# Optimization experiments

Measured on AMD Instinct MI355X. Metric: run time of the kernel, lower is better.

Reference implementation:

```python
import jax, jax.numpy as jnp
import numpy as np
from jax import lax

B, T, I, H, L = 64, 2048, 128, 256, 2
P = 0.25  # dropouto


def _lstm_layer(x, W_ih, W_hh, b_ih, b_hh):
    """Single LSTM layer. x: [B,T,in]. Torch gate order: i, f, g, o."""
    # Precompute input projection for all timesteps (one big GEMM).
    xW = jnp.einsum('bti,gi->btg', x, W_ih) + b_ih + b_hh  # [B,T,4H]
    h0 = jnp.zeros((x.shape[0], W_hh.shape[1]), x.dtype)
    c0 = jnp.zeros_like(h0)

    def step(carry, xw_t):
        h, c = carry
        g = xw_t + h @ W_hh.T  # [B,4H]
        i, f, gg, o = jnp.split(g, 4, axis=-1)
        c = jax.nn.sigmoid(f) * c + jax.nn.sigmoid(i) * jnp.tanh(gg)
        h = jax.nn.sigmoid(o) * jnp.tanh(c)
        return (h, c), h

    (hT, cT), hs = lax.scan(step, (h0, c0), xW.transpose(1, 0, 2))
    return hs.transpose(1, 0, 2), hT, cT  # [B,T,H], [B,H], [B,H]


def setup_inputs() -> dict:
    key = jax.random.key(0)
    ks = jax.random.split(key, 16)
    s = 1.0 / np.sqrt(H)
    inp = {'x': jax.random.normal(ks[0], (B, T, I), jnp.float32)}
    for l in range(L):
        d_in = I if l == 0 else H
        inp[f'W_ih{l}'] = jax.random.uniform(ks[1 + 4 * l], (4 * H, d_in), jnp.float32, -s, s)
        inp[f'W_hh{l}'] = jax.random.uniform(ks[2 + 4 * l], (4 * H, H), jnp.float32, -s, s)
        inp[f'b_ih{l}'] = jax.random.uniform(ks[3 + 4 * l], (4 * H,), jnp.float32, -s, s)
        inp[f'b_hh{l}'] = jax.random.uniform(ks[4 + 4 * l], (4 * H,), jnp.float32, -s, s)
        # variational dropout mask on layer output: same mask for every timestep
        keep = jax.random.bernoulli(ks[9 + l], 1.0 - P, (B, H))
        inp[f'mask{l}'] = keep.astype(jnp.float32) / (1.0 - P)
    return inp


def reference(x, W_ih0, W_hh0, b_ih0, b_hh0, W_ih1, W_hh1, b_ih1, b_hh1, mask0, mask1):
    params = [(W_ih0, W_hh0, b_ih0, b_hh0, mask0), (W_ih1, W_hh1, b_ih1, b_hh1, mask1)]
    h_ns, c_ns = [], []
    out = x
    for (W_ih, W_hh, b_ih, b_hh, mask) in params:
        out, hT, cT = _lstm_layer(out, W_ih, W_hh, b_ih, b_hh)
        out = out * mask[:, None, :]  # variational dropouto (shared over time)
        h_ns.append(hT)
        c_ns.append(cT)
    h_n = jnp.stack(h_ns, axis=0)  # [L,B,H]
    c_n = jnp.stack(c_ns, axis=0)
    return out, (h_n, c_n)
```

## Files before the change

### kernel.cpp

```cpp
#include <hip/hip_runtime.h>

#define B_  64
#define T_  2048
#define I_  128
#define H_  256
#define G4  1024
#define TC  128

#define HC  16
#define MC  9
#define SC  7

typedef float    f32x4 __attribute__((ext_vector_type(4)));
typedef _Float16 f16x8 __attribute__((ext_vector_type(8)));
typedef _Float16 f16x2 __attribute__((ext_vector_type(2)));

__device__ __forceinline__ float dot2f(unsigned w, unsigned h, float acc) {
#if __has_builtin(__builtin_amdgcn_fdot2)
  return __builtin_amdgcn_fdot2(__builtin_bit_cast(f16x2, w),
                                __builtin_bit_cast(f16x2, h), acc, false);
#else
  f16x2 a = __builtin_bit_cast(f16x2, w), b = __builtin_bit_cast(f16x2, h);
  return acc + (float)a[0] * (float)b[0] + (float)a[1] * (float)b[1];
#endif
}

__device__ __forceinline__ unsigned short h16bits(float f) {
  return __builtin_bit_cast(unsigned short, (_Float16)f);
}
__device__ __forceinline__ float sigm(float x) { return 1.f / (1.f + __expf(-x)); }
__device__ __forceinline__ float tanh_fast(float x) { return 2.f / (1.f + __expf(-2.f * x)) - 1.f; }


__global__ void prep_w(const float* __restrict__ Whh, uint4* __restrict__ wall) {
  int idx = blockIdx.x * 256 + threadIdx.x;
  if (idx >= 32 * 1024) return;
  int c4 = idx >> 10, r = idx & 1023;
  unsigned q[4];
#pragma unroll
  for (int m = 0; m < 4; m++) {
    int kd = 4 * c4 + m;
    unsigned lo = h16bits(Whh[r * 256 + 2 * kd]);
    unsigned hi = h16bits(Whh[r * 256 + 2 * kd + 1]);
    q[m] = lo | (hi << 16);
  }
  wall[c4 * 1024 + r] = make_uint4(q[0], q[1], q[2], q[3]);
}

__global__ void prep_f16(const float* __restrict__ src, _Float16* __restrict__ dst, int n) {
  int i = blockIdx.x * 256 + threadIdx.x;
  if (i < n) dst[i] = (_Float16)src[i];
}

__global__ void prep_bias(const float* __restrict__ bi, const float* __restrict__ bh,
                          float* __restrict__ bias) {
  int i = blockIdx.x * 256 + threadIdx.x;
  if (i < G4) bias[i] = bi[i] + bh[i];
}

template <int K, bool SRC_F32>
__global__ __launch_bounds__(256) void proj_kernel(const void* __restrict__ Asrc,
                                                   const _Float16* __restrict__ Wf,
                                                   const float* __restrict__ bias,
                                                   _Float16* __restrict__ xw, int t0) {
  const int m  = blockIdx.x;
  const int n0 = blockIdx.y * 64;
  const int tid = threadIdx.x;
  const int lane = tid & 63, wv = tid >> 6;

  __shared__ _Float16 As[64][40];
  __shared__ _Float16 Bs[64][40];

  f32x4 acc[4] = {f32x4{0,0,0,0}, f32x4{0,0,0,0}, f32x4{0,0,0,0}, f32x4{0,0,0,0}};

  const int r  = tid >> 2;
  const int kq = (tid & 3) * 8;
  const int r_g = m * 64 + r;
  const int b  = r_g >> 7;
  const int tc = r_g & (TC - 1);
  long arow;
  if (SRC_F32) arow = (long)(b * T_ + t0 + tc) * K;
  else         arow = (long)r_g * K;

  for (int k0 = 0; k0 < K; k0 += 32) {
    if (SRC_F32) {
      const float* ap = (const float*)Asrc + arow + k0 + kq;
      float4 a0 = *(const float4*)ap;
      float4 a1 = *(const float4*)(ap + 4);
      _Float16* d = &As[r][kq];
      d[0] = (_Float16)a0.x; d[1] = (_Float16)a0.y; d[2] = (_Float16)a0.z; d[3] = (_Float16)a0.w;
      d[4] = (_Float16)a1.x; d[5] = (_Float16)a1.y; d[6] = (_Float16)a1.z; d[7] = (_Float16)a1.w;
    } else {
      const _Float16* ap = (const _Float16*)Asrc + arow + k0 + kq;
      *(uint4*)&As[r][kq] = *(const uint4*)ap;
    }
    *(uint4*)&Bs[r][kq] = *(const uint4*)(Wf + (long)(n0 + r) * K + k0 + kq);
    __syncthreads();

    f16x8 av = *(const f16x8*)&As[wv * 16 + (lane & 15)][(lane >> 4) * 8];
#pragma unroll
    for (int q = 0; q < 4; q++) {
      f16x8 bv = *(const f16x8*)&Bs[q * 16 + (lane & 15)][(lane >> 4) * 8];
      acc[q] = __builtin_amdgcn_mfma_f32_16x16x32_f16(av, bv, acc[q], 0, 0, 0);
    }
    __syncthreads();
  }

  const int row_in = wv * 16 + ((lane >> 4) << 2);
  const int col_in = lane & 15;
#pragma unroll
  for (int q = 0; q < 4; q++) {
#pragma unroll
    for (int i = 0; i < 4; i++) {
      int rr = m * 64 + row_in + i;
      int cc = n0 + q * 16 + col_in;
      xw[(long)rr * G4 + cc] = (_Float16)(acc[q][i] + bias[cc]);
    }
  }
}


struct ScanJob {
  const _Float16* xw;
  const uint4*    wall;
  const float*    mask;
  float* hstate; float* cstate;
  _Float16* ychunk;
  float* out;
  float* hn; float* cn;
  int t0; int valid;
};

#define C16(X) X(0) X(1) X(2) X(3) X(4) X(5) X(6) X(7) \
               X(8) X(9) X(10) X(11) X(12) X(13) X(14) X(15)

#define LOADW(i) \
  uint4 wA_##i = wall[(i) * 1024 + r0]; \
  uint4 wB_##i = wall[(i) * 1024 + r1];

#define PINW(i) \
  asm volatile("" : "+v"(wA_##i.x), "+v"(wA_##i.y), "+v"(wA_##i.z), "+v"(wA_##i.w), \
                    "+v"(wB_##i.x), "+v"(wB_##i.y), "+v"(wB_##i.z), "+v"(wB_##i.w));

#define DOTW(i) { uint4 hv = hs4[i]; \
  accA0 = dot2f(wA_##i.x, hv.x, accA0); accB0 = dot2f(wB_##i.x, hv.x, accB0); \
  accA1 = dot2f(wA_##i.y, hv.y, accA1); accB1 = dot2f(wB_##i.y, hv.y, accB1); \
  accA0 = dot2f(wA_##i.z, hv.z, accA0); accB0 = dot2f(wB_##i.z, hv.z, accB0); \
  accA1 = dot2f(wA_##i.w, hv.w, accA1); accB1 = dot2f(wB_##i.w, hv.w, accB1); }

__global__ __launch_bounds__(512)
__attribute__((amdgpu_waves_per_eu(2, 2)))
void scan_kernel(ScanJob j0, ScanJob j1) {
  ScanJob j = (blockIdx.x < B_) ? j0 : j1;
  if (!j.valid) return;
  const int b = blockIdx.x & (B_ - 1);
  const int t = threadIdx.x;
  const int p = t & 255, s = t >> 8;
  const int r0 = p + s * 256;
  const int r1 = r0 + 512;

  __shared__ uint4 wmid[MC * 1024];
  __shared__ __align__(16) unsigned short hsm[256];
  __shared__ float pig[256];

  const uint4* wall = j.wall;

#pragma unroll
  for (int i = 0; i < MC * 2; i++)
    wmid[i * 512 + t] = wall[HC * 1024 + i * 512 + t];

  C16(LOADW)
  C16(PINW)

  float c_reg = 0.f, h_reg = 0.f, mk = 0.f;
  if (s == 1) {
    c_reg = j.cstate[b * 256 + p];
    mk    = j.mask[b * 256 + p];
  }
  if (t < 128) {
    float h0v = j.hstate[b * 256 + 2 * t];
    float h1v = j.hstate[b * 256 + 2 * t + 1];
    ((unsigned*)hsm)[t] = (unsigned)h16bits(h0v) | ((unsigned)h16bits(h1v) << 16);
  }
  __syncthreads();

  const uint4* hs4 = (const uint4*)hsm;
  const _Float16* xwb = j.xw + (long)b * TC * G4;
  float xA = (float)xwb[r0], xB = (float)xwb[r1];
  float hm_prev = 0.f;

  for (int tc = 0; tc < TC; ++tc) {
    float nA = 0.f, nB = 0.f;
    if (tc + 1 < TC) {
      nA = (float)xwb[(long)(tc + 1) * G4 + r0];
      nB = (float)xwb[(long)(tc + 1) * G4 + r1];
    }

    if (s == 1 && tc > 0) {
      if (j.ychunk) j.ychunk[(b * TC + tc - 1) * H_ + p] = (_Float16)hm_prev;
      else          j.out[(long)(b * T_ + j.t0 + tc - 1) * H_ + p] = hm_prev;
    }

    float accA0 = xA, accA1 = 0.f, accB0 = xB, accB1 = 0.f;

    {
      const uint4* wsp = wall + (HC + MC) * 1024;
      asm volatile("" : "+v"(wsp));
#pragma unroll
      for (int m = 0; m < SC; m++) {
        uint4 hv = hs4[HC + MC + m];
        uint4 gA = wsp[m * 1024 + r0];
        uint4 gB = wsp[m * 1024 + r1];
        accA0 = dot2f(gA.x, hv.x, accA0); accB0 = dot2f(gB.x, hv.x, accB0);
        accA1 = dot2f(gA.y, hv.y, accA1); accB1 = dot2f(gB.y, hv.y, accB1);
        accA0 = dot2f(gA.z, hv.z, accA0); accB0 = dot2f(gB.z, hv.z, accB0);
        accA1 = dot2f(gA.w, hv.w, accA1); accB1 = dot2f(gB.w, hv.w, accB1);
      }
    }

    C16(DOTW)

#pragma unroll
    for (int m = 0; m < MC; m++) {
      uint4 hv = hs4[HC + m];
      uint4 tA = wmid[m * 1024 + r0];
      uint4 tB = wmid[m * 1024 + r1];
      accA0 = dot2f(tA.x, hv.x, accA0); accB0 = dot2f(tB.x, hv.x, accB0);
      accA1 = dot2f(tA.y, hv.y, accA1); accB1 = dot2f(tB.y, hv.y, accB1);
      accA0 = dot2f(tA.z, hv.z, accA0); accB0 = dot2f(tB.z, hv.z, accB0);
      accA1 = dot2f(tA.w, hv.w, accA1); accB1 = dot2f(tB.w, hv.w, accB1);
    }

    float aF = accA0 + accA1;
    float bF = accB0 + accB1;

    if (s == 0) pig[p] = sigm(aF) * tanh_fast(bF);
    __syncthreads();
    if (s == 1) {
      c_reg = sigm(aF) * c_reg + pig[p];
      h_reg = sigm(bF) * tanh_fast(c_reg);
      hsm[p] = h16bits(h_reg);
      hm_prev = h_reg * mk;
    }
    xA = nA; xB = nB;
    __syncthreads();
  }

  if (s == 1) {
    if (j.ychunk) j.ychunk[(b * TC + TC - 1) * H_ + p] = (_Float16)hm_prev;
    else          j.out[(long)(b * T_ + j.t0 + TC - 1) * H_ + p] = hm_prev;
    j.hstate[b * 256 + p] = h_reg;
    j.cstate[b * 256 + p] = c_reg;
    if (j.hn) { j.hn[b * 256 + p] = h_reg; j.cn[b * 256 + p] = c_reg; }
  }
}

extern "C" void kernel_launch(void* const* d_in, const int* in_sizes, int n_in,
                              void* d_out, int out_size, void* d_ws, size_t ws_size,
                              hipStream_t stream) {
  const float* x     = (const float*)d_in[0];
  const float* Wih0  = (const float*)d_in[1];
  const float* Whh0  = (const float*)d_in[2];
  const float* bih0  = (const float*)d_in[3];
  const float* bhh0  = (const float*)d_in[4];
  const float* mask0 = (const float*)d_in[5];
  const float* Wih1  = (const float*)d_in[6];
  const float* Whh1  = (const float*)d_in[7];
  const float* bih1  = (const float*)d_in[8];
  const float* bhh1  = (const float*)d_in[9];
  const float* mask1 = (const float*)d_in[10];

  float* out = (float*)d_out;
  float* hn  = out + (long)B_ * T_ * H_;
  float* cn  = hn + 2 * B_ * H_;

  char* w = (char*)d_ws;
  uint4*    wall0  = (uint4*)w;      w += 512 << 10;
  uint4*    wall1  = (uint4*)w;      w += 512 << 10;
  _Float16* wf0    = (_Float16*)w;   w += 256 << 10;
  _Float16* wf1    = (_Float16*)w;   w += 512 << 10;
  float*    bias0  = (float*)w;      w += 4 << 10;
  float*    bias1  = (float*)w;      w += 4 << 10;
  float*    h0s    = (float*)w;      w += 64 << 10;
  float*    c0s    = (float*)w;      w += 64 << 10;
  float*    h1s    = (float*)w;      w += 64 << 10;
  float*    c1s    = (float*)w;      w += 64 << 10;
  _Float16* xw0    = (_Float16*)w;   w += (long)B_ * TC * G4 * 2;
  _Float16* xw1    = (_Float16*)w;   w += (long)B_ * TC * G4 * 2;
  _Float16* ybuf   = (_Float16*)w;   w += (long)B_ * TC * H_ * 2;

  hipMemsetAsync(h0s, 0, 4 * (64 << 10), stream);

  prep_w<<<128, 256, 0, stream>>>(Whh0, wall0);
  prep_w<<<128, 256, 0, stream>>>(Whh1, wall1);
  prep_f16<<<512, 256, 0, stream>>>(Wih0, wf0, G4 * I_);
  prep_f16<<<1024, 256, 0, stream>>>(Wih1, wf1, G4 * H_);
  prep_bias<<<4, 256, 0, stream>>>(bih0, bhh0, bias0);
  prep_bias<<<4, 256, 0, stream>>>(bih1, bhh1, bias1);

  const int nchunk = T_ / TC;
  for (int k = 0; k <= nchunk; k++) {
    if (k < nchunk) {
      proj_kernel<I_, true><<<dim3(B_ * TC / 64, G4 / 64), 256, 0, stream>>>(
          x, wf0, bias0, xw0, k * TC);
    }
    ScanJob j0, j1;
    j0.xw = xw0; j0.wall = wall0; j0.mask = mask0;
    j0.hstate = h0s; j0.cstate = c0s;
    j0.ychunk = ybuf; j0.out = nullptr;
    j0.hn = (k == nchunk - 1) ? hn : nullptr;
    j0.cn = (k == nchunk - 1) ? cn : nullptr;
    j0.t0 = k * TC; j0.valid = (k < nchunk);
    j1.xw = xw1; j1.wall = wall1; j1.mask = mask1;
    j1.hstate = h1s; j1.cstate = c1s;
    j1.ychunk = nullptr; j1.out = out;
    j1.hn = (k == nchunk) ? hn + B_ * H_ : nullptr;
    j1.cn = (k == nchunk) ? cn + B_ * H_ : nullptr;
    j1.t0 = (k - 1) * TC; j1.valid = (k >= 1);

    scan_kernel<<<2 * B_, 512, 0, stream>>>(j0, j1);

    if (k < nchunk) {
      proj_kernel<H_, false><<<dim3(B_ * TC / 64, G4 / 64), 256, 0, stream>>>(
          ybuf, wf1, bias1, xw1, k * TC);
    }
  }
}
```

Baseline: 6.372 ms.

## Process two batch rows per scan block to share recurrent weight loads

Each scan block now runs the recurrence for two batch rows at once, so every weight fragment it loads is used against two hidden-state vectors. The grid is halved to one block per batch pair. The weight split also changes: fewer chunks stay pinned in registers (HC from 16 to 8) and more are streamed from global memory, interleaved with software-prefetched loads. The trade is more arithmetic and more global/L2 weight traffic per timestep on each block, with only half as many CUs active, in exchange for reusing each weight across two batches.

```diff
diff --git a/kernel.cpp b/kernel.cpp
--- a/kernel.cpp
+++ b/kernel.cpp
@@ -7,9 +7,8 @@
 #define G4  1024
 #define TC  128
 
-#define HC  16
+#define HC  8
 #define MC  9
-#define SC  7
 
 typedef float    f32x4 __attribute__((ext_vector_type(4)));
 typedef _Float16 f16x8 __attribute__((ext_vector_type(8)));
@@ -131,127 +130,152 @@
   int t0; int valid;
 };
 
-#define C16(X) X(0) X(1) X(2) X(3) X(4) X(5) X(6) X(7) \
-               X(8) X(9) X(10) X(11) X(12) X(13) X(14) X(15)
+#define C8(X) X(0) X(1) X(2) X(3) X(4) X(5) X(6) X(7)
 
 #define LOADW(i) \
-  uint4 wA_##i = wall[(i) * 1024 + r0]; \
-  uint4 wB_##i = wall[(i) * 1024 + r1];
+  uint4 wA_##i = wall_p[(i) * 1024 + r0]; \
+  uint4 wB_##i = wall_p[(i) * 1024 + r1];
 
 #define PINW(i) \
   asm volatile("" : "+v"(wA_##i.x), "+v"(wA_##i.y), "+v"(wA_##i.z), "+v"(wA_##i.w), \
                     "+v"(wB_##i.x), "+v"(wB_##i.y), "+v"(wB_##i.z), "+v"(wB_##i.w));
 
-#define DOTW(i) { uint4 hv = hs4[i]; \
-  accA0 = dot2f(wA_##i.x, hv.x, accA0); accB0 = dot2f(wB_##i.x, hv.x, accB0); \
-  accA1 = dot2f(wA_##i.y, hv.y, accA1); accB1 = dot2f(wB_##i.y, hv.y, accB1); \
-  accA0 = dot2f(wA_##i.z, hv.z, accA0); accB0 = dot2f(wB_##i.z, hv.z, accB0); \
-  accA1 = dot2f(wA_##i.w, hv.w, accA1); accB1 = dot2f(wB_##i.w, hv.w, accB1); }
-
-__global__ __launch_bounds__(512)
-__attribute__((amdgpu_waves_per_eu(2, 2)))
-void scan_kernel(ScanJob j0, ScanJob j1) {
-  ScanJob j = (blockIdx.x < B_) ? j0 : j1;
+#define DOT2T(gA, gB, c) { uint4 hv0 = hsA[c]; uint4 hv1 = hsB[c]; \
+  a00 = dot2f(gA.x, hv0.x, a00); a10 = dot2f(gA.x, hv1.x, a10); \
+  a01 = dot2f(gB.x, hv0.x, a01); a11 = dot2f(gB.x, hv1.x, a11); \
+  a00 = dot2f(gA.y, hv0.y, a00); a10 = dot2f(gA.y, hv1.y, a10); \
+  a01 = dot2f(gB.y, hv0.y, a01); a11 = dot2f(gB.y, hv1.y, a11); \
+  a00 = dot2f(gA.z, hv0.z, a00); a10 = dot2f(gA.z, hv1.z, a10); \
+  a01 = dot2f(gB.z, hv0.z, a01); a11 = dot2f(gB.z, hv1.z, a11); \
+  a00 = dot2f(gA.w, hv0.w, a00); a10 = dot2f(gA.w, hv1.w, a10); \
+  a01 = dot2f(gB.w, hv0.w, a01); a11 = dot2f(gB.w, hv1.w, a11); }
+
+#define DOTR(i)   DOT2T(wA_##i, wB_##i, i)
+#define DOTL(c)   { uint4 tA = wmid[((c) - HC) * 1024 + r0]; \
+                    uint4 tB = wmid[((c) - HC) * 1024 + r1]; \
+                    DOT2T(tA, tB, c) }
+#define LOADS(n, c) uint4 sA_##n = wsp[((c) - HC - MC) * 1024 + r0]; \
+                    uint4 sB_##n = wsp[((c) - HC - MC) * 1024 + r1];
+#define DOTS(n, c)  DOT2T(sA_##n, sB_##n, c)
+
+__global__ __launch_bounds__(512, 1) void scan_kernel(ScanJob j0, ScanJob j1) {
+  const int nb = gridDim.x >> 1;
+  ScanJob j = (blockIdx.x < nb) ? j0 : j1;
   if (!j.valid) return;
-  const int b = blockIdx.x & (B_ - 1);
+  const int bb = (blockIdx.x < nb) ? blockIdx.x : blockIdx.x - nb;
+  const int b0 = 2 * bb, b1 = 2 * bb + 1;
   const int t = threadIdx.x;
-  const int p = t & 255, s = t >> 8;
-  const int r0 = p + s * 256;
-  const int r1 = r0 + 512;
+  const int r0 = t, r1 = t + 512;
+  const int s = t >> 8, jj = t & 255;
 
   __shared__ uint4 wmid[MC * 1024];
-  __shared__ __align__(16) unsigned short hsm[256];
-  __shared__ float pig[256];
-
-  const uint4* wall = j.wall;
+  __shared__ __align__(16) unsigned short hsm[2][256];
+  __shared__ float pig[2][256];
+
+  const uint4* wall_p = j.wall;
 
 #pragma unroll
   for (int i = 0; i < MC * 2; i++)
-    wmid[i * 512 + t] = wall[HC * 1024 + i * 512 + t];
-
-  C16(LOADW)
-  C16(PINW)
-
-  float c_reg = 0.f, h_reg = 0.f, mk = 0.f;
+    wmid[i * 512 + t] = wall_p[HC * 1024 + i * 512 + t];
+
+  C8(LOADW)
+  C8(PINW)
+
+  float c0 = 0.f, c1 = 0.f, h0 = 0.f, h1 = 0.f, mk0 = 0.f, mk1 = 0.f;
   if (s == 1) {
-    c_reg = j.cstate[b * 256 + p];
-    mk    = j.mask[b * 256 + p];
-  }
-  if (t < 128) {
-    float h0v = j.hstate[b * 256 + 2 * t];
-    float h1v = j.hstate[b * 256 + 2 * t + 1];
-    ((unsigned*)hsm)[t] = (unsigned)h16bits(h0v) | ((unsigned)h16bits(h1v) << 16);
+    c0  = j.cstate[b0 * 256 + jj];
+    c1  = j.cstate[b1 * 256 + jj];
+    mk0 = j.mask[b0 * 256 + jj];
+    mk1 = j.mask[b1 * 256 + jj];
+    hsm[1][jj] = h16bits(j.hstate[b1 * 256 + jj]);
+  } else {
+    hsm[0][jj] = h16bits(j.hstate[b0 * 256 + jj]);
   }
   __syncthreads();
 
-  const uint4* hs4 = (const uint4*)hsm;
-  const _Float16* xwb = j.xw + (long)b * TC * G4;
-  float xA = (float)xwb[r0], xB = (float)xwb[r1];
-  float hm_prev = 0.f;
+  const uint4* hsA = (const uint4*)hsm[0];
+  const uint4* hsB = (const uint4*)hsm[1];
+  const _Float16* xwb0 = j.xw + (long)b0 * TC * G4;
+  const _Float16* xwb1 = j.xw + (long)b1 * TC * G4;
+  float x00 = (float)xwb0[r0], x01 = (float)xwb0[r1];
+  float x10 = (float)xwb1[r0], x11 = (float)xwb1[r1];
+  float hm0p = 0.f, hm1p = 0.f;
 
   for (int tc = 0; tc < TC; ++tc) {
-    float nA = 0.f, nB = 0.f;
+    float n00 = 0.f, n01 = 0.f, n10 = 0.f, n11 = 0.f;
     if (tc + 1 < TC) {
-      nA = (float)xwb[(long)(tc + 1) * G4 + r0];
-      nB = (float)xwb[(long)(tc + 1) * G4 + r1];
+      const long nx = (long)(tc + 1) * G4;
+      n00 = (float)xwb0[nx + r0]; n01 = (float)xwb0[nx + r1];
+      n10 = (float)xwb1[nx + r0]; n11 = (float)xwb1[nx + r1];
     }
 
     if (s == 1 && tc > 0) {
-      if (j.ychunk) j.ychunk[(b * TC + tc - 1) * H_ + p] = (_Float16)hm_prev;
-      else          j.out[(long)(b * T_ + j.t0 + tc - 1) * H_ + p] = hm_prev;
-    }
-
-    float accA0 = xA, accA1 = 0.f, accB0 = xB, accB1 = 0.f;
-
-    {
-      const uint4* wsp = wall + (HC + MC) * 1024;
-      asm volatile("" : "+v"(wsp));
-#pragma unroll
-      for (int m = 0; m < SC; m++) {
-        uint4 hv = hs4[HC + MC + m];
-        uint4 gA = wsp[m * 1024 + r0];
-        uint4 gB = wsp[m * 1024 + r1];
-        accA0 = dot2f(gA.x, hv.x, accA0); accB0 = dot2f(gB.x, hv.x, accB0);
-        accA1 = dot2f(gA.y, hv.y, accA1); accB1 = dot2f(gB.y, hv.y, accB1);
-        accA0 = dot2f(gA.z, hv.z, accA0); accB0 = dot2f(gB.z, hv.z, accB0);
-        accA1 = dot2f(gA.w, hv.w, accA1); accB1 = dot2f(gB.w, hv.w, accB1);
+      if (j.ychunk) {
+        j.ychunk[(b0 * TC + tc - 1) * H_ + jj] = (_Float16)hm0p;
+        j.ychunk[(b1 * TC + tc - 1) * H_ + jj] = (_Float16)hm1p;
+      } else {
+        j.out[(long)(b0 * T_ + j.t0 + tc - 1) * H_ + jj] = hm0p;
+        j.out[(long)(b1 * T_ + j.t0 + tc - 1) * H_ + jj] = hm1p;
       }
     }
 
-    C16(DOTW)
-
-#pragma unroll
-    for (int m = 0; m < MC; m++) {
-      uint4 hv = hs4[HC + m];
-      uint4 tA = wmid[m * 1024 + r0];
-      uint4 tB = wmid[m * 1024 + r1];
-      accA0 = dot2f(tA.x, hv.x, accA0); accB0 = dot2f(tB.x, hv.x, accB0);
-      accA1 = dot2f(tA.y, hv.y, accA1); accB1 = dot2f(tB.y, hv.y, accB1);
-      accA0 = dot2f(tA.z, hv.z, accA0); accB0 = dot2f(tB.z, hv.z, accB0);
-      accA1 = dot2f(tA.w, hv.w, accA1); accB1 = dot2f(tB.w, hv.w, accB1);
-    }
-
-    float aF = accA0 + accA1;
-    float bF = accB0 + accB1;
-
-    if (s == 0) pig[p] = sigm(aF) * tanh_fast(bF);
+    float a00 = x00, a01 = x01, a10 = x10, a11 = x11;
+
+    const uint4* wsp = wall_p + (HC + MC) * 1024;
+    asm volatile("" : "+v"(wsp));
+
+    LOADS(0, 17) LOADS(1, 18) LOADS(2, 19) LOADS(3, 20)
+    C8(DOTR)
+    DOTS(0, 17) DOTS(1, 18)
+
+    LOADS(4, 21) LOADS(5, 22) LOADS(6, 23) LOADS(7, 24)
+    DOTS(2, 19) DOTS(3, 20)
+    DOTL(8) DOTL(9) DOTL(10)
+    DOTS(4, 21) DOTS(5, 22)
+
+    LOADS(8, 25) LOADS(9, 26) LOADS(10, 27) LOADS(11, 28)
+    DOTS(6, 23) DOTS(7, 24)
+    DOTL(11) DOTL(12) DOTL(13)
+    DOTS(8, 25) DOTS(9, 26)
+
+    LOADS(12, 29) LOADS(13, 30) LOADS(14, 31)
+    DOTS(10, 27) DOTS(11, 28)
+    DOTL(14) DOTL(15) DOTL(16)
+    DOTS(12, 29) DOTS(13, 30) DOTS(14, 31)
+
+    if (s == 0) {
+      pig[0][jj] = sigm(a00) * tanh_fast(a01);
+      pig[1][jj] = sigm(a10) * tanh_fast(a11);
+    }
     __syncthreads();
     if (s == 1) {
-      c_reg = sigm(aF) * c_reg + pig[p];
-      h_reg = sigm(bF) * tanh_fast(c_reg);
-      hsm[p] = h16bits(h_reg);
-      hm_prev = h_reg * mk;
-    }
-    xA = nA; xB = nB;
+      c0 = sigm(a00) * c0 + pig[0][jj];
+      h0 = sigm(a01) * tanh_fast(c0);
+      hsm[0][jj] = h16bits(h0);
+      hm0p = h0 * mk0;
+      c1 = sigm(a10) * c1 + pig[1][jj];
+      h1 = sigm(a11) * tanh_fast(c1);
+      hsm[1][jj] = h16bits(h1);
+      hm1p = h1 * mk1;
+    }
+    x00 = n00; x01 = n01; x10 = n10; x11 = n11;
     __syncthreads();
   }
 
   if (s == 1) {
-    if (j.ychunk) j.ychunk[(b * TC + TC - 1) * H_ + p] = (_Float16)hm_prev;
-    else          j.out[(long)(b * T_ + j.t0 + TC - 1) * H_ + p] = hm_prev;
-    j.hstate[b * 256 + p] = h_reg;
-    j.cstate[b * 256 + p] = c_reg;
-    if (j.hn) { j.hn[b * 256 + p] = h_reg; j.cn[b * 256 + p] = c_reg; }
+    if (j.ychunk) {
+      j.ychunk[(b0 * TC + TC - 1) * H_ + jj] = (_Float16)hm0p;
+      j.ychunk[(b1 * TC + TC - 1) * H_ + jj] = (_Float16)hm1p;
+    } else {
+      j.out[(long)(b0 * T_ + j.t0 + TC - 1) * H_ + jj] = hm0p;
+      j.out[(long)(b1 * T_ + j.t0 + TC - 1) * H_ + jj] = hm1p;
+    }
+    j.hstate[b0 * 256 + jj] = h0; j.cstate[b0 * 256 + jj] = c0;
+    j.hstate[b1 * 256 + jj] = h1; j.cstate[b1 * 256 + jj] = c1;
+    if (j.hn) {
+      j.hn[b0 * 256 + jj] = h0; j.cn[b0 * 256 + jj] = c0;
+      j.hn[b1 * 256 + jj] = h1; j.cn[b1 * 256 + jj] = c1;
+    }
   }
 }
 
@@ -318,7 +342,7 @@
     j1.cn = (k == nchunk) ? cn + B_ * H_ : nullptr;
     j1.t0 = (k - 1) * TC; j1.valid = (k >= 1);
 
-    scan_kernel<<<2 * B_, 512, 0, stream>>>(j0, j1);
+    scan_kernel<<<B_, 512, 0, stream>>>(j0, j1);
 
     if (k < nchunk) {
       proj_kernel<H_, false><<<dim3(B_ * TC / 64, G4 / 64), 256, 0, stream>>>(
```

Result: slower. 9.039 ms (+41.9%).

## Keep 23 weight chunks in registers, drop per-step global weight streaming

Applied to the files above, without the earlier changes.

Moves the seven recurrent-weight chunks that were re-read from global or L2 memory every timestep into registers, growing the register-resident set from 16 to 23 uint4 pairs. Launch bounds change to one block per CU, replacing the waves-per-EU hint so the larger register budget is allowed. The goal is to remove per-step global loads from the serial recurrence critical path. The risk is register pressure and spilling, since each thread now pins 184 VGPRs of weights.

```diff
diff --git a/kernel.cpp b/kernel.cpp
--- a/kernel.cpp
+++ b/kernel.cpp
@@ -7,9 +7,8 @@
 #define G4  1024
 #define TC  128
 
-#define HC  16
+#define HC  23
 #define MC  9
-#define SC  7
 
 typedef float    f32x4 __attribute__((ext_vector_type(4)));
 typedef _Float16 f16x8 __attribute__((ext_vector_type(8)));
@@ -131,26 +130,26 @@
   int t0; int valid;
 };
 
-#define C16(X) X(0) X(1) X(2) X(3) X(4) X(5) X(6) X(7) \
-               X(8) X(9) X(10) X(11) X(12) X(13) X(14) X(15)
+#define C23(X) X(0) X(1) X(2) X(3) X(4) X(5) X(6) X(7) X(8) X(9) X(10) X(11) \
+               X(12) X(13) X(14) X(15) X(16) X(17) X(18) X(19) X(20) X(21) X(22)
 
 #define LOADW(i) \
-  uint4 wA_##i = wall[(i) * 1024 + r0]; \
-  uint4 wB_##i = wall[(i) * 1024 + r1];
+  uint4 wA_##i = wall_p[(i) * 1024 + r0]; \
+  uint4 wB_##i = wall_p[(i) * 1024 + r1];
 
 #define PINW(i) \
   asm volatile("" : "+v"(wA_##i.x), "+v"(wA_##i.y), "+v"(wA_##i.z), "+v"(wA_##i.w), \
                     "+v"(wB_##i.x), "+v"(wB_##i.y), "+v"(wB_##i.z), "+v"(wB_##i.w));
 
-#define DOTW(i) { uint4 hv = hs4[i]; \
-  accA0 = dot2f(wA_##i.x, hv.x, accA0); accB0 = dot2f(wB_##i.x, hv.x, accB0); \
-  accA1 = dot2f(wA_##i.y, hv.y, accA1); accB1 = dot2f(wB_##i.y, hv.y, accB1); \
-  accA0 = dot2f(wA_##i.z, hv.z, accA0); accB0 = dot2f(wB_##i.z, hv.z, accB0); \
-  accA1 = dot2f(wA_##i.w, hv.w, accA1); accB1 = dot2f(wB_##i.w, hv.w, accB1); }
-
-__global__ __launch_bounds__(512)
-__attribute__((amdgpu_waves_per_eu(2, 2)))
-void scan_kernel(ScanJob j0, ScanJob j1) {
+#define DOT2(gA, gB, c) { uint4 hv = hs4[c]; \
+  a0 = dot2f(gA.x, hv.x, a0); a1 = dot2f(gB.x, hv.x, a1); \
+  b0 = dot2f(gA.y, hv.y, b0); b1 = dot2f(gB.y, hv.y, b1); \
+  a0 = dot2f(gA.z, hv.z, a0); a1 = dot2f(gB.z, hv.z, a1); \
+  b0 = dot2f(gA.w, hv.w, b0); b1 = dot2f(gB.w, hv.w, b1); }
+
+#define DOTR(i)  DOT2(wA_##i, wB_##i, i)
+
+__global__ __launch_bounds__(512, 1) void scan_kernel(ScanJob j0, ScanJob j1) {
   ScanJob j = (blockIdx.x < B_) ? j0 : j1;
   if (!j.valid) return;
   const int b = blockIdx.x & (B_ - 1);
@@ -163,24 +162,21 @@
   __shared__ __align__(16) unsigned short hsm[256];
   __shared__ float pig[256];
 
-  const uint4* wall = j.wall;
+  const uint4* wall_p = j.wall;
 
 #pragma unroll
   for (int i = 0; i < MC * 2; i++)
-    wmid[i * 512 + t] = wall[HC * 1024 + i * 512 + t];
-
-  C16(LOADW)
-  C16(PINW)
+    wmid[i * 512 + t] = wall_p[HC * 1024 + i * 512 + t];
+
+  C23(LOADW)
+  C23(PINW)
 
   float c_reg = 0.f, h_reg = 0.f, mk = 0.f;
   if (s == 1) {
     c_reg = j.cstate[b * 256 + p];
     mk    = j.mask[b * 256 + p];
-  }
-  if (t < 128) {
-    float h0v = j.hstate[b * 256 + 2 * t];
-    float h1v = j.hstate[b * 256 + 2 * t + 1];
-    ((unsigned*)hsm)[t] = (unsigned)h16bits(h0v) | ((unsigned)h16bits(h1v) << 16);
+  } else {
+    hsm[p] = h16bits(j.hstate[b * 256 + p]);
   }
   __syncthreads();
 
@@ -201,38 +197,19 @@
       else          j.out[(long)(b * T_ + j.t0 + tc - 1) * H_ + p] = hm_prev;
     }
 
-    float accA0 = xA, accA1 = 0.f, accB0 = xB, accB1 = 0.f;
-
-    {
-      const uint4* wsp = wall + (HC + MC) * 1024;
-      asm volatile("" : "+v"(wsp));
-#pragma unroll
-      for (int m = 0; m < SC; m++) {
-        uint4 hv = hs4[HC + MC + m];
-        uint4 gA = wsp[m * 1024 + r0];
-        uint4 gB = wsp[m * 1024 + r1];
-        accA0 = dot2f(gA.x, hv.x, accA0); accB0 = dot2f(gB.x, hv.x, accB0);
-        accA1 = dot2f(gA.y, hv.y, accA1); accB1 = dot2f(gB.y, hv.y, accB1);
-        accA0 = dot2f(gA.z, hv.z, accA0); accB0 = dot2f(gB.z, hv.z, accB0);
-        accA1 = dot2f(gA.w, hv.w, accA1); accB1 = dot2f(gB.w, hv.w, accB1);
-      }
-    }
-
-    C16(DOTW)
+    float a0 = xA, a1 = xB, b0 = 0.f, b1 = 0.f;
+
+    C23(DOTR)
 
 #pragma unroll
     for (int m = 0; m < MC; m++) {
-      uint4 hv = hs4[HC + m];
       uint4 tA = wmid[m * 1024 + r0];
       uint4 tB = wmid[m * 1024 + r1];
-      accA0 = dot2f(tA.x, hv.x, accA0); accB0 = dot2f(tB.x, hv.x, accB0);
-      accA1 = dot2f(tA.y, hv.y, accA1); accB1 = dot2f(tB.y, hv.y, accB1);
-      accA0 = dot2f(tA.z, hv.z, accA0); accB0 = dot2f(tB.z, hv.z, accB0);
-      accA1 = dot2f(tA.w, hv.w, accA1); accB1 = dot2f(tB.w, hv.w, accB1);
-    }
-
-    float aF = accA0 + accA1;
-    float bF = accB0 + accB1;
+      DOT2(tA, tB, HC + m)
+    }
+
+    float aF = a0 + b0;
+    float bF = a1 + b1;
 
     if (s == 0) pig[p] = sigm(aF) * tanh_fast(bF);
     __syncthreads();
```

After: 5.336 ms, median of 2. -16.2%, faster.
